# Kernel optimization log

Hardware: AMD Instinct MI355X
Metric: run time of the kernel (lower is better)

## Reference

```python
import jax, jax.numpy as jnp
import numpy as np

N_NODES = 100000
N_FEAT = 128
N_EDGES = 600000


def setup_inputs() -> dict:
    key = jax.random.key(0)
    k1, k2, k3, k4 = jax.random.split(key, 4)
    return {
        "input": jax.random.normal(k1, (N_NODES, N_FEAT), dtype=jnp.float32),
        "sidx": jax.random.randint(k2, (N_EDGES,), 0, N_NODES),
        "tidx": jax.random.randint(k3, (N_EDGES,), 0, N_NODES),
        "enorm": jax.random.uniform(k4, (N_EDGES,), dtype=jnp.float32),
        "esgn": jnp.ones((N_EDGES,), dtype=jnp.float32),
    }


def reference(input, sidx, tidx, enorm, esgn):
    # message[e] = input[sidx[e]] * (esgn[e] * enorm[e])  -> scatter-add into tidx
    message = input[sidx] * (esgn * enorm)[:, None]  # [E, F]
    res = jax.ops.segment_sum(message, tidx, num_segments=input.shape[0])
    return res.astype(input.dtype)
```

## Files before the change

### kernel.cpp

```cpp
#include <hip/hip_runtime.h>
#include <hip/hip_bf16.h>


#define NCHUNK 256
#define BSHIFT 6
#define BNODES 64
#define NCAP   24
#define MAXB   2048

typedef float f32x2 __attribute__((ext_vector_type(2)));
typedef float f32x4 __attribute__((ext_vector_type(4)));

struct Ovf { int t; int src; float w; };

__device__ __forceinline__ unsigned bf16rne(float f) {
    unsigned u = __builtin_bit_cast(unsigned, f);
    return (u + 0x7FFFu + ((u >> 16) & 1u)) >> 16;
}

__device__ __forceinline__ void push_ovf(Ovf* ovf, int* ovf_count, int ovf_cap,
                                         int t, int s, float w) {
    const int o = atomicAdd(ovf_count, 1);
    if (o < ovf_cap) { Ovf v; v.t = t; v.src = s; v.w = w; ovf[o] = v; }
}

__global__ __launch_bounds__(256)
void build_convert(const int* __restrict__ tidx,
                   const int* __restrict__ sidx,
                   const float* __restrict__ enorm,
                   const float* __restrict__ esgn,
                   int* __restrict__ subcnt,
                   int* __restrict__ suboff,
                   unsigned long long* __restrict__ records,
                   int n_edges, int nbuckets, int epc,
                   const float* __restrict__ input,
                   unsigned* __restrict__ input_bf,
                   int n_cvt8) {
    if ((int)blockIdx.x < NCHUNK) {
        __shared__ int s_cnt[MAXB];
        __shared__ int s_off[MAXB];
        __shared__ int s_part[256];
        const int chunk = blockIdx.x;
        const int tid   = threadIdx.x;

        for (int i = tid; i < nbuckets; i += 256) s_cnt[i] = 0;
        __syncthreads();

        const int e0 = chunk * epc;
        const int e1 = min(e0 + epc, n_edges);
        for (int e = e0 + tid; e < e1; e += 256)
            atomicAdd(&s_cnt[tidx[e] >> BSHIFT], 1);
        __syncthreads();

        int local[8];
        int sum = 0;
        #pragma unroll
        for (int k = 0; k < 8; ++k) {
            const int idx = tid * 8 + k;
            local[k] = (idx < nbuckets) ? s_cnt[idx] : 0;
            sum += local[k];
        }
        s_part[tid] = sum;
        __syncthreads();
        for (int d = 1; d < 256; d <<= 1) {
            const int v = (tid >= d) ? s_part[tid - d] : 0;
            __syncthreads();
            s_part[tid] += v;
            __syncthreads();
        }
        int run = s_part[tid] - sum;
        #pragma unroll
        for (int k = 0; k < 8; ++k) {
            const int idx = tid * 8 + k;
            if (idx < nbuckets) { s_off[idx] = run; run += local[k]; }
        }
        __syncthreads();

        for (int i = tid; i < nbuckets; i += 256) {
            subcnt[(size_t)i * NCHUNK + chunk] = s_cnt[i];
            suboff[(size_t)i * NCHUNK + chunk] = s_off[i];
            s_cnt[i] = 0;
        }
        __syncthreads();

        const size_t base = (size_t)chunk * epc;
        for (int e = e0 + tid; e < e1; e += 256) {
            const int t  = tidx[e];
            const int b  = t >> BSHIFT;
            const int tl = t & (BNODES - 1);
            const unsigned meta = (unsigned)sidx[e] | ((unsigned)tl << 17);
            const float w = esgn[e] * enorm[e];
            const int slot = atomicAdd(&s_cnt[b], 1);
            records[base + s_off[b] + slot] =
                (unsigned long long)meta |
                ((unsigned long long)__builtin_bit_cast(unsigned, w) << 32);
        }
    } else {
        const int c = ((int)blockIdx.x - NCHUNK) * (int)blockDim.x + (int)threadIdx.x;
        if (c < n_cvt8) {
            const f32x4 a = __builtin_nontemporal_load(
                reinterpret_cast<const f32x4*>(input + (size_t)c * 8));
            const f32x4 b = __builtin_nontemporal_load(
                reinterpret_cast<const f32x4*>(input + (size_t)c * 8 + 4));
            uint4 p;
            p.x = bf16rne(a.x) | (bf16rne(a.y) << 16);
            p.y = bf16rne(a.z) | (bf16rne(a.w) << 16);
            p.z = bf16rne(b.x) | (bf16rne(b.y) << 16);
            p.w = bf16rne(b.z) | (bf16rne(b.w) << 16);
            *reinterpret_cast<uint4*>(input_bf + (size_t)c * 4) = p;
        }
    }
}

__global__ __launch_bounds__(256)
void bucket_gather(const int* __restrict__ subcnt,
                   const int* __restrict__ suboff,
                   const unsigned long long* __restrict__ records,
                   const unsigned* __restrict__ input_bf,
                   float* __restrict__ out,
                   Ovf* __restrict__ ovf,
                   int* __restrict__ ovf_count,
                   int ovf_cap,
                   int n_nodes, int epc) {
    __shared__ int      s_segoff[NCHUNK];
    __shared__ int      s_pref[NCHUNK + 1];
    __shared__ int      s_ncnt[BNODES];
    __shared__ unsigned s_rec[BNODES][NCAP];

    const int b    = blockIdx.x;
    const int tid  = threadIdx.x;
    const int lane = tid & 63;
    const int wv   = tid >> 6;

    if (tid < BNODES) s_ncnt[tid] = 0;
    s_segoff[tid] = suboff[(size_t)b * NCHUNK + tid];

    const int mycnt = subcnt[(size_t)b * NCHUNK + tid];
    s_pref[tid + 1] = mycnt;
    if (tid == 0) s_pref[0] = 0;
    __syncthreads();
    for (int d = 1; d < 256; d <<= 1) {
        const int v = (tid + 1 > d) ? s_pref[tid + 1 - d] : 0;
        __syncthreads();
        s_pref[tid + 1] += v;
        __syncthreads();
    }

    const int total = s_pref[NCHUNK];
    for (int i = tid; i < total; i += 256) {
        int lo = 0, hi = NCHUNK - 1;
        while (lo < hi) {
            const int mid = (lo + hi + 1) >> 1;
            if (s_pref[mid] <= i) lo = mid; else hi = mid - 1;
        }
        const unsigned long long rec =
            records[(size_t)lo * epc + s_segoff[lo] + (i - s_pref[lo])];
        const unsigned meta = (unsigned)rec;
        const int   src = (int)(meta & 0x1FFFFu);
        const int   tl  = (int)(meta >> 17) & (BNODES - 1);
        const float w   = __builtin_bit_cast(float, (unsigned)(rec >> 32));
        const int slot = atomicAdd(&s_ncnt[tl], 1);
        const bool ok  = (w >= 0.f) && (w < 1.f);
        if (slot < NCAP) {
            unsigned word = 0u;
            if (ok) {
                unsigned wq = (unsigned)(w * 32768.f + 0.5f);
                if (wq > 32767u) wq = 32767u;
                word = ((unsigned)src << 15) | wq;
            }
            s_rec[tl][slot] = word;
            if (!ok) push_ovf(ovf, ovf_count, ovf_cap, b * BNODES + tl, src, w);
        } else {
            push_ovf(ovf, ovf_count, ovf_cap, b * BNODES + tl, src, w);
        }
    }
    __syncthreads();

    for (int base = wv; base < BNODES; base += 8) {
        const int nlA = base;
        const int nlB = base + 4;
        const int nodeA = b * BNODES + nlA;
        const int nodeB = b * BNODES + nlB;
        const int cntA = (nodeA < n_nodes) ? min(s_ncnt[nlA], NCAP) : 0;
        const int cntB = (nodeB < n_nodes) ? min(s_ncnt[nlB], NCAP) : 0;
        const int cmax = max(cntA, cntB);

        float2 a0 = make_float2(0.f, 0.f), a1 = make_float2(0.f, 0.f);
        float2 b0 = make_float2(0.f, 0.f), b1 = make_float2(0.f, 0.f);

        for (int j = 0; j < cmax; j += 4) {
            if (j < cntA) {
                unsigned rc[4], v[4];
                float    wq[4];
                #pragma unroll
                for (int k = 0; k < 4; ++k) {
                    const int jk = min(j + k, cntA - 1);
                    rc[k] = s_rec[nlA][jk];
                    wq[k] = (j + k < cntA)
                          ? (float)(rc[k] & 0x7FFFu) * (1.f / 32768.f) : 0.f;
                }
                #pragma unroll
                for (int k = 0; k < 4; ++k)
                    v[k] = input_bf[(size_t)(rc[k] >> 15) * 64 + lane];
                #pragma unroll
                for (int k = 0; k < 4; k += 2) {
                    a0.x += __builtin_bit_cast(float, v[k] << 16) * wq[k];
                    a0.y += __builtin_bit_cast(float, v[k] & 0xFFFF0000u) * wq[k];
                    a1.x += __builtin_bit_cast(float, v[k+1] << 16) * wq[k+1];
                    a1.y += __builtin_bit_cast(float, v[k+1] & 0xFFFF0000u) * wq[k+1];
                }
            }
            if (j < cntB) {
                unsigned rc[4], v[4];
                float    wq[4];
                #pragma unroll
                for (int k = 0; k < 4; ++k) {
                    const int jk = min(j + k, cntB - 1);
                    rc[k] = s_rec[nlB][jk];
                    wq[k] = (j + k < cntB)
                          ? (float)(rc[k] & 0x7FFFu) * (1.f / 32768.f) : 0.f;
                }
                #pragma unroll
                for (int k = 0; k < 4; ++k)
                    v[k] = input_bf[(size_t)(rc[k] >> 15) * 64 + lane];
                #pragma unroll
                for (int k = 0; k < 4; k += 2) {
                    b0.x += __builtin_bit_cast(float, v[k] << 16) * wq[k];
                    b0.y += __builtin_bit_cast(float, v[k] & 0xFFFF0000u) * wq[k];
                    b1.x += __builtin_bit_cast(float, v[k+1] << 16) * wq[k+1];
                    b1.y += __builtin_bit_cast(float, v[k+1] & 0xFFFF0000u) * wq[k+1];
                }
            }
        }

        if (nodeA < n_nodes) {
            f32x2 r; r.x = a0.x + a1.x; r.y = a0.y + a1.y;
            __builtin_nontemporal_store(r,
                reinterpret_cast<f32x2*>(out + (size_t)nodeA * 128 + lane * 2));
        }
        if (nodeB < n_nodes) {
            f32x2 r; r.x = b0.x + b1.x; r.y = b0.y + b1.y;
            __builtin_nontemporal_store(r,
                reinterpret_cast<f32x2*>(out + (size_t)nodeB * 128 + lane * 2));
        }
    }
}

__global__ void fixup_ovf(const float* __restrict__ input,
                          const Ovf* __restrict__ ovf,
                          const int* __restrict__ ovf_count,
                          float* __restrict__ out,
                          int ovf_cap) {
    const int n = min(*ovf_count, ovf_cap);
    const int wave   = (blockIdx.x * blockDim.x + threadIdx.x) >> 6;
    const int lane   = threadIdx.x & 63;
    const int nwaves = (gridDim.x * blockDim.x) >> 6;
    for (int i = wave; i < n; i += nwaves) {
        const Ovf o = ovf[i];
        const float2 v = *reinterpret_cast<const float2*>(input + (size_t)(o.src * 128 + lane * 2));
        float* dst = out + (size_t)(o.t * 128 + lane * 2);
        atomicAdd(dst + 0, v.x * o.w);
        atomicAdd(dst + 1, v.y * o.w);
    }
}

__global__ void graphconv_scatter(const float* __restrict__ input,
                                  const int* __restrict__ sidx,
                                  const int* __restrict__ tidx,
                                  const float* __restrict__ enorm,
                                  const float* __restrict__ esgn,
                                  float* __restrict__ out,
                                  int n_edges) {
    const int gtid   = blockIdx.x * blockDim.x + threadIdx.x;
    const int wave   = gtid >> 6;
    const int lane   = threadIdx.x & 63;
    const int nwaves = (gridDim.x * blockDim.x) >> 6;
    for (int e = wave; e < n_edges; e += nwaves) {
        const float w = esgn[e] * enorm[e];
        const float2 v = *reinterpret_cast<const float2*>(input + (size_t)(sidx[e] * 128 + lane * 2));
        float* dst = out + (size_t)(tidx[e] * 128 + lane * 2);
        atomicAdd(dst + 0, v.x * w);
        atomicAdd(dst + 1, v.y * w);
    }
}

extern "C" void kernel_launch(void* const* d_in, const int* in_sizes, int n_in,
                              void* d_out, int out_size, void* d_ws, size_t ws_size,
                              hipStream_t stream) {
    const float* input = (const float*)d_in[0];
    const int*   sidx  = (const int*)d_in[1];
    const int*   tidx  = (const int*)d_in[2];
    const float* enorm = (const float*)d_in[3];
    const float* esgn  = (const float*)d_in[4];
    float*       out   = (float*)d_out;

    const int n_edges  = in_sizes[1];
    const int n_nodes  = in_sizes[0] / 128;
    const int n_elem   = in_sizes[0];
    const int nbuckets = (n_nodes + BNODES - 1) >> BSHIFT;
    const int epc      = (n_edges + NCHUNK - 1) / NCHUNK;

    const size_t tbl_ints  = (size_t)nbuckets * NCHUNK;
    const size_t hdr_bytes = (2 * tbl_ints + 1) * sizeof(int);
    const size_t rec_off   = (hdr_bytes + 255) & ~(size_t)255;
    const size_t rec_bytes = (size_t)NCHUNK * epc * sizeof(unsigned long long);
    const size_t bf_off    = rec_off + rec_bytes;
    const size_t bf_bytes  = (size_t)n_elem * 2;
    const size_t ovf_off   = bf_off + bf_bytes;
    const size_t min_ovf   = 4096 * sizeof(Ovf);

    if (nbuckets > MAXB || n_nodes > (1 << 17) || ws_size < ovf_off + min_ovf) {
        (void)hipMemsetAsync(d_out, 0, (size_t)out_size * sizeof(float), stream);
        int grid = (n_edges * 64 + 255) / 256;
        if (grid > 2048) grid = 2048;
        graphconv_scatter<<<grid, 256, 0, stream>>>(input, sidx, tidx, enorm, esgn,
                                                    out, n_edges);
        return;
    }

    int*      subcnt    = (int*)d_ws;
    int*      suboff    = subcnt + tbl_ints;
    int*      ovf_count = suboff + tbl_ints;
    unsigned long long* records = (unsigned long long*)((char*)d_ws + rec_off);
    unsigned* input_bf  = (unsigned*)((char*)d_ws + bf_off);
    Ovf*      ovf       = (Ovf*)((char*)d_ws + ovf_off);
    int       ovf_cap   = (int)((ws_size - ovf_off) / sizeof(Ovf));
    if (ovf_cap > n_edges) ovf_cap = n_edges;

    (void)hipMemsetAsync(ovf_count, 0, sizeof(int), stream);

    const int block = 256;
    const int n_cvt8 = n_elem / 8;
    const int cvt_blocks = (n_cvt8 + block - 1) / block;

    build_convert<<<NCHUNK + cvt_blocks, block, 0, stream>>>(
        tidx, sidx, enorm, esgn, subcnt, suboff, records,
        n_edges, nbuckets, epc, input, input_bf, n_cvt8);

    bucket_gather<<<nbuckets, block, 0, stream>>>(
        subcnt, suboff, records, input_bf, out, ovf, ovf_count, ovf_cap,
        n_nodes, epc);

    fixup_ovf<<<32, block, 0, stream>>>(input, ovf, ovf_count, out, ovf_cap);
}
```

Baseline: 72.69 us.

## Gather four nodes per wave iteration and fold overflow counter reset into kernel

The gather loop now has each wave process four nodes per iteration instead of two, so up to sixteen independent bf16 row loads are in flight before the accumulations. This raises memory-level parallelism at the cost of more registers. The separate memset of the overflow counter is removed and its reset moved into the first block of build_convert, saving one stream operation. The first record slot of each node is also zero-initialised so the clamped index reads defined data.

```diff
diff --git a/kernel.cpp b/kernel.cpp
--- a/kernel.cpp
+++ b/kernel.cpp
@@ -32,6 +32,7 @@
                    int* __restrict__ subcnt,
                    int* __restrict__ suboff,
                    unsigned long long* __restrict__ records,
+                   int* __restrict__ ovf_count,
                    int n_edges, int nbuckets, int epc,
                    const float* __restrict__ input,
                    unsigned* __restrict__ input_bf,
@@ -42,6 +43,8 @@
         __shared__ int s_part[256];
         const int chunk = blockIdx.x;
         const int tid   = threadIdx.x;
+
+        if (chunk == 0 && tid == 0) *ovf_count = 0;
 
         for (int i = tid; i < nbuckets; i += 256) s_cnt[i] = 0;
         __syncthreads();
@@ -132,7 +135,7 @@
     const int lane = tid & 63;
     const int wv   = tid >> 6;
 
-    if (tid < BNODES) s_ncnt[tid] = 0;
+    if (tid < BNODES) { s_ncnt[tid] = 0; s_rec[tid][0] = 0u; }
     s_segoff[tid] = suboff[(size_t)b * NCHUNK + tid];
 
     const int mycnt = subcnt[(size_t)b * NCHUNK + tid];
@@ -176,72 +179,71 @@
     }
     __syncthreads();
 
-    for (int base = wv; base < BNODES; base += 8) {
-        const int nlA = base;
-        const int nlB = base + 4;
-        const int nodeA = b * BNODES + nlA;
-        const int nodeB = b * BNODES + nlB;
-        const int cntA = (nodeA < n_nodes) ? min(s_ncnt[nlA], NCAP) : 0;
-        const int cntB = (nodeB < n_nodes) ? min(s_ncnt[nlB], NCAP) : 0;
-        const int cmax = max(cntA, cntB);
-
-        float2 a0 = make_float2(0.f, 0.f), a1 = make_float2(0.f, 0.f);
-        float2 b0 = make_float2(0.f, 0.f), b1 = make_float2(0.f, 0.f);
+    for (int base = wv; base < BNODES; base += 16) {
+        int nl[4], cnt[4];
+        #pragma unroll
+        for (int q = 0; q < 4; ++q) {
+            nl[q] = base + q * 4;
+            const int node = b * BNODES + nl[q];
+            cnt[q] = (node < n_nodes) ? min(s_ncnt[nl[q]], NCAP) : 0;
+        }
+        const int cmax = max(max(cnt[0], cnt[1]), max(cnt[2], cnt[3]));
+
+        f32x2 acc0[4], acc1[4];
+        #pragma unroll
+        for (int q = 0; q < 4; ++q) {
+            acc0[q] = (f32x2){0.f, 0.f};
+            acc1[q] = (f32x2){0.f, 0.f};
+        }
 
         for (int j = 0; j < cmax; j += 4) {
-            if (j < cntA) {
-                unsigned rc[4], v[4];
-                float    wq[4];
-                #pragma unroll
-                for (int k = 0; k < 4; ++k) {
-                    const int jk = min(j + k, cntA - 1);
-                    rc[k] = s_rec[nlA][jk];
-                    wq[k] = (j + k < cntA)
-                          ? (float)(rc[k] & 0x7FFFu) * (1.f / 32768.f) : 0.f;
+            unsigned rc[4][4], v[4][4];
+            float    wq[4][4];
+            #pragma unroll
+            for (int q = 0; q < 4; ++q) {
+                if (j < cnt[q]) {
+                    #pragma unroll
+                    for (int k = 0; k < 4; ++k) {
+                        const int jk = min(j + k, cnt[q] - 1);
+                        rc[q][k] = s_rec[nl[q]][jk];
+                        wq[q][k] = (j + k < cnt[q])
+                                 ? (float)(rc[q][k] & 0x7FFFu) * (1.f / 32768.f)
+                                 : 0.f;
+                    }
                 }
-                #pragma unroll
-                for (int k = 0; k < 4; ++k)
-                    v[k] = input_bf[(size_t)(rc[k] >> 15) * 64 + lane];
-                #pragma unroll
-                for (int k = 0; k < 4; k += 2) {
-                    a0.x += __builtin_bit_cast(float, v[k] << 16) * wq[k];
-                    a0.y += __builtin_bit_cast(float, v[k] & 0xFFFF0000u) * wq[k];
-                    a1.x += __builtin_bit_cast(float, v[k+1] << 16) * wq[k+1];
-                    a1.y += __builtin_bit_cast(float, v[k+1] & 0xFFFF0000u) * wq[k+1];
+            }
+            #pragma unroll
+            for (int q = 0; q < 4; ++q) {
+                if (j < cnt[q]) {
+                    #pragma unroll
+                    for (int k = 0; k < 4; ++k)
+                        v[q][k] = input_bf[(size_t)(rc[q][k] >> 15) * 64 + lane];
                 }
             }
-            if (j < cntB) {
-                unsigned rc[4], v[4];
-                float    wq[4];
-                #pragma unroll
-                for (int k = 0; k < 4; ++k) {
-                    const int jk = min(j + k, cntB - 1);
-                    rc[k] = s_rec[nlB][jk];
-                    wq[k] = (j + k < cntB)
-                          ? (float)(rc[k] & 0x7FFFu) * (1.f / 32768.f) : 0.f;
+            #pragma unroll
+            for (int q = 0; q < 4; ++q) {
+                if (j < cnt[q]) {
+                    #pragma unroll
+                    for (int k = 0; k < 4; k += 2) {
+                        acc0[q].x += __builtin_bit_cast(float, v[q][k] << 16) * wq[q][k];
+                        acc0[q].y += __builtin_bit_cast(float, v[q][k] & 0xFFFF0000u) * wq[q][k];
+                        acc1[q].x += __builtin_bit_cast(float, v[q][k+1] << 16) * wq[q][k+1];
+                        acc1[q].y += __builtin_bit_cast(float, v[q][k+1] & 0xFFFF0000u) * wq[q][k+1];
+                    }
                 }
-                #pragma unroll
-                for (int k = 0; k < 4; ++k)
-                    v[k] = input_bf[(size_t)(rc[k] >> 15) * 64 + lane];
-                #pragma unroll
-                for (int k = 0; k < 4; k += 2) {
-                    b0.x += __builtin_bit_cast(float, v[k] << 16) * wq[k];
-                    b0.y += __builtin_bit_cast(float, v[k] & 0xFFFF0000u) * wq[k];
-                    b1.x += __builtin_bit_cast(float, v[k+1] << 16) * wq[k+1];
-                    b1.y += __builtin_bit_cast(float, v[k+1] & 0xFFFF0000u) * wq[k+1];
-                }
-            }
-        }
-
-        if (nodeA < n_nodes) {
-            f32x2 r; r.x = a0.x + a1.x; r.y = a0.y + a1.y;
-            __builtin_nontemporal_store(r,
-                reinterpret_cast<f32x2*>(out + (size_t)nodeA * 128 + lane * 2));
-        }
-        if (nodeB < n_nodes) {
-            f32x2 r; r.x = b0.x + b1.x; r.y = b0.y + b1.y;
-            __builtin_nontemporal_store(r,
-                reinterpret_cast<f32x2*>(out + (size_t)nodeB * 128 + lane * 2));
+            }
+        }
+
+        #pragma unroll
+        for (int q = 0; q < 4; ++q) {
+            const int node = b * BNODES + nl[q];
+            if (node < n_nodes) {
+                f32x2 r;
+                r.x = acc0[q].x + acc1[q].x;
+                r.y = acc0[q].y + acc1[q].y;
+                __builtin_nontemporal_store(r,
+                    reinterpret_cast<f32x2*>(out + (size_t)node * 128 + lane * 2));
+            }
         }
     }
 }
@@ -327,14 +329,12 @@
     int       ovf_cap   = (int)((ws_size - ovf_off) / sizeof(Ovf));
     if (ovf_cap > n_edges) ovf_cap = n_edges;
 
-    (void)hipMemsetAsync(ovf_count, 0, sizeof(int), stream);
-
     const int block = 256;
     const int n_cvt8 = n_elem / 8;
     const int cvt_blocks = (n_cvt8 + block - 1) / block;
 
     build_convert<<<NCHUNK + cvt_blocks, block, 0, stream>>>(
-        tidx, sidx, enorm, esgn, subcnt, suboff, records,
+        tidx, sidx, enorm, esgn, subcnt, suboff, records, ovf_count,
         n_edges, nbuckets, epc, input, input_bf, n_cvt8);
 
     bucket_gather<<<nbuckets, block, 0, stream>>>(
```

New measurement: 81.54 us. +12.2%, slower.
